# Kernel tuning notes

Hardware: AMD Instinct MI355X
Metric: run time of the kernel (lower is better)

Reference implementation:

```python
import jax, jax.numpy as jnp
import numpy as np

H_STEP = 0.1  # diffusion step size h


def vector_layer(V, W):
    """V: [B, Cin, 9, N]; W: [Cout, Cin, 6].
    Faithful to torch vectorLayer: per component-group, conv1d with kernel
    covering the 3 group entries == contraction over (Cin, group), then the
    scalar result is broadcast back to the 3 group positions.
    Groups [0,3,6]->W[:,:,:3], [1,4,7]->W[:,:,3:6], [2,5,8]->W[:,:,3:6]."""
    o0 = jnp.einsum('bcgn,ocg->bon', V[:, :, (0, 3, 6), :], W[:, :, 0:3])
    o1 = jnp.einsum('bcgn,ocg->bon', V[:, :, (1, 4, 7), :], W[:, :, 3:6])
    o2 = jnp.einsum('bcgn,ocg->bon', V[:, :, (2, 5, 8), :], W[:, :, 3:6])
    S = jnp.stack([o0, o1, o2], axis=2)          # [B, Cout, 3, N]
    return jnp.tile(S, (1, 1, 3, 1))             # positions i get o_{i%3}


def vector_relu(V, Q):
    """Projection ReLU. V: [B, C, 9, N] viewed as [B, C, 3, 3(xyz), N];
    subtract the ReLU'd projection onto direction Q per 3-vector."""
    B, C, _, N = V.shape
    V5 = V.reshape(B, C, 3, 3, N)
    qnorm = jnp.linalg.norm(Q)
    Qb = (Q / qnorm)[None, None, None, :, None]
    T = jnp.sum(V5 * Q[None, None, None, :, None], axis=3, keepdims=True)
    W = V5 - jax.nn.relu(T / qnorm) * Qb
    return W.reshape(B, C, 9, N)


def double_vector_layer(x, K1, K2, Q):
    x = vector_relu(x, Q)
    x = vector_layer(x, K1)
    x = vector_relu(x, Q)
    x = vector_layer(x, K2)
    return vector_relu(x, Q)


def setup_inputs() -> dict:
    key = jax.random.key(0)
    ks = jax.random.split(key, 12)
    N, E = 8192, 65536
    nNin, nEin, nNopen, nEopen, nNclose, nlayer = 3, 1, 16, 1, 3, 5
    nopen = nNopen + 2 * nEopen   # 18
    nhid = 2 * nopen              # 36
    s = 0.05  # kernel scale for numerical stability over 5 layers
    return {
        'xnV': jax.random.normal(ks[0], (1, nNin, 9, N), jnp.float32),
        'xeV': jax.random.normal(ks[1], (1, nEin, 9, E), jnp.float32),
        'iInd': jax.random.randint(ks[2], (E,), 0, N),
        'jInd': jax.random.randint(ks[3], (E,), 0, N),
        'K1Nopen': s * jax.random.normal(ks[4], (nNopen, nNin, 6), jnp.float32),
        'K2Nopen': s * jax.random.normal(ks[5], (nNopen, nNopen, 6), jnp.float32),
        'K1Eopen': s * jax.random.normal(ks[6], (nEopen, nEin, 6), jnp.float32),
        'K2Eopen': s * jax.random.normal(ks[7], (nEopen, nEopen, 6), jnp.float32),
        'KE1': s * jax.random.normal(ks[8], (nlayer, nhid, nhid, 6), jnp.float32),
        'KE2': s * jax.random.normal(ks[9], (nlayer, nhid, nhid, 6), jnp.float32),
        'KNclose': s * jax.random.normal(ks[10], (nNclose, nopen, 6), jnp.float32),
        'Q': jax.random.normal(ks[11], (3,), jnp.float32),
    }


def reference(xnV, xeV, iInd, jInd, K1Nopen, K2Nopen, K1Eopen, K2Eopen,
              KE1, KE2, KNclose, Q):
    N = xnV.shape[-1]
    nopen = K2Nopen.shape[0] + 2 * K2Eopen.shape[0]

    def node_grad(x):   # node -> edge gather difference
        return x[..., iInd] - x[..., jInd]

    def node_ave(x):    # node -> edge gather average
        return 0.5 * (x[..., iInd] + x[..., jInd])

    def edge_div(g):    # edge -> node signed scatter-add
        z = jnp.zeros(g.shape[:-1] + (N,), g.dtype)
        return z.at[..., iInd].add(g).at[..., jInd].add(-g)

    def edge_ave(g):    # edge -> node averaged scatter-add
        z = jnp.zeros(g.shape[:-1] + (N,), g.dtype)
        return 0.5 * z.at[..., iInd].add(g).at[..., jInd].add(g)

    xn = double_vector_layer(xnV, K1Nopen, K2Nopen, Q)   # [1,16,9,N]
    xe = double_vector_layer(xeV, K1Eopen, K2Eopen, Q)   # [1,1,9,E]
    xn = jnp.concatenate([xn, edge_div(xe), edge_ave(xe)], axis=1)  # [1,18,9,N]

    Flux = None
    for i in range(KE1.shape[0]):  # fixed nlayer=5 structurally distinct weights
        dxe = jnp.concatenate([node_grad(xn), node_ave(xn)], axis=1)  # [1,36,9,E]
        Flux = double_vector_layer(dxe, KE1[i], KE2[i], Q)            # [1,36,9,E]
        dxn = edge_div(Flux[:, :nopen]) + edge_ave(Flux[:, nopen:])   # [1,18,9,N]
        xn = xn - H_STEP * dxn

    out = vector_layer(xn, KNclose)  # [1,3,9,N]
    return out, Flux
```

## Files before the change

### kernel.cpp

```cpp
#include <hip/hip_runtime.h>

#define N_NODES 8192
#define N_EDGES 65536
#define NS 56

#define XN3_OFF   0
#define MIT_OFF   (N_NODES*NS)
#define K2N_OFF   (MIT_OFF + 5*5760)
#define KNC_OFF   (K2N_OFF + 2*16*16)
#define K2E_OFF   (KNC_OFF + 2*3*18)
#define FLUX_OFF  488176
#define FLUX_END  (FLUX_OFF + 2*N_EDGES*32)
#define DEG_OFF   FLUX_END
#define RP_OFF    (DEG_OFF + N_NODES)
#define FP_OFF    (RP_OFF + N_NODES + 1)
#define POSI_OFF  (FP_OFF + N_NODES)
#define POSJ_OFF  (POSI_OFF + N_EDGES)

typedef float f32x2 __attribute__((ext_vector_type(2)));
typedef __fp16 fp16x2 __attribute__((ext_vector_type(2)));

__device__ __forceinline__ unsigned pkrtz(float a, float b) {
    fp16x2 h = __builtin_amdgcn_cvt_pkrtz(a, b);
    return *(unsigned*)&h;
}

template<int SLOT>
__device__ __forceinline__ float qb(float x) {
    int r = __builtin_amdgcn_update_dpp(0, __float_as_int(x), SLOT * 0x55, 0xf, 0xf, true);
    return __int_as_float(r);
}
__device__ __forceinline__ float qswap2(float x) {
    int r = __builtin_amdgcn_update_dpp(0, __float_as_int(x), 0x4E, 0xf, 0xf, true);
    return __int_as_float(r);
}

__device__ __forceinline__ void vrelu_p(float& a0, f32x2& a12,
                                        float q0, f32x2 q12, float iq2) {
    float t = fmaf(a0, q0, fmaf(a12.x, q12.x, a12.y * q12.y));
    float r = t > 0.f ? t * iq2 : 0.f;
    a0 = fmaf(-r, q0, a0);
    f32x2 nr = {-r, -r};
    a12 = nr * q12 + a12;
}

__device__ __forceinline__ void vrelu3(float& x0, float& x1, float& x2,
                                       float q0, float q1, float q2, float iq2) {
    float t = x0*q0 + x1*q1 + x2*q2;
    float r = t > 0.f ? t*iq2 : 0.f;
    x0 = fmaf(-r, q0, x0);
    x1 = fmaf(-r, q1, x1);
    x2 = fmaf(-r, q2, x2);
}

template<int QS>
__device__ __forceinline__ void matvec_part(const float* __restrict__ mbase, int q,
        const float (&v0)[9], const f32x2 (&v12)[9],
        f32x2 (&a0p)[4], float& a0s, f32x2 (&a12)[9]) {
    const float* rb = mbase + QS*720 + q*20;
#pragma unroll
    for (int kc = 0; kc < 9; ++kc) {
        float b0 = qb<QS>(v0[kc]);
        f32x2 b12; b12.x = qb<QS>(v12[kc].x); b12.y = qb<QS>(v12[kc].y);
        f32x2 bb0 = {b0, b0};
        const float4* rp = (const float4*)(rb + kc*80);
        float4 R0 = rp[0], R1 = rp[1], R2 = rp[2], R3 = rp[3], R4 = rp[4];
        f32x2 m0p[4] = {{R0.x,R0.y},{R0.z,R0.w},{R1.x,R1.y},{R1.z,R1.w}};
        float mA[9] = {R2.z,R2.w,R3.x,R3.y,R3.z,R3.w,R4.x,R4.y,R4.z};
#pragma unroll
        for (int k = 0; k < 4; ++k) a0p[k] = m0p[k] * bb0 + a0p[k];
        a0s = fmaf(R2.x, b0, a0s);
#pragma unroll
        for (int k = 0; k < 9; ++k) {
            f32x2 mm = {mA[k], mA[k]};
            a12[k] = mm * b12 + a12[k];
        }
    }
}

__global__ void precompute_kernel(const float* __restrict__ K2N,
                                  const float* __restrict__ K2E,
                                  const float* __restrict__ KE1,
                                  const float* __restrict__ KE2,
                                  const float* __restrict__ KNc,
                                  float* __restrict__ ws,
                                  int* __restrict__ deg) {
    int tid = blockIdx.x * blockDim.x + threadIdx.x;
    int nthr = gridDim.x * blockDim.x;
    if (tid < N_NODES) deg[tid] = 0;
    for (int m = tid; m < 1440; m += nthr) {
        ws[MIT_OFF + m*20 + 9]  = 0.f;
        ws[MIT_OFF + m*20 + 19] = 0.f;
    }
    for (int m = tid; m < 5*1296; m += nthr) {
        int l = m / 1296, oc = m % 1296;
        int o = oc / 36, c = oc % 36;
        int qq = o / 9, k = o % 9;
        const float* p1 = KE1 + (size_t)(l*1296 + oc)*6;
        const float* p2 = KE2 + (size_t)(l*1296 + oc)*6;
        int base = MIT_OFF + l*5760 + (c*4 + qq)*20;
        ws[base + k]             = p1[0] + p1[1] + p1[2];
        ws[base + 10 + k]        = p1[3] + p1[4] + p1[5];
        ws[base + 2880 + k]      = p2[0] + p2[1] + p2[2];
        ws[base + 2880 + 10 + k] = p2[3] + p2[4] + p2[5];
    }
    for (int m = tid; m < 2*256; m += nthr) {
        int s = m / 256, oc = m % 256;
        const float* p = K2N + oc*6 + 3*s;
        ws[K2N_OFF + m] = p[0] + p[1] + p[2];
    }
    for (int m = tid; m < 2*54; m += nthr) {
        int s = m / 54, oc = m % 54;
        const float* p = KNc + oc*6 + 3*s;
        ws[KNC_OFF + m] = p[0] + p[1] + p[2];
    }
    if (tid < 2) {
        const float* p = K2E + 3*tid;
        ws[K2E_OFF + tid] = p[0] + p[1] + p[2];
    }
}

__global__ void count_kernel(const int* __restrict__ iInd, const int* __restrict__ jInd,
                             int* __restrict__ deg) {
    int e = blockIdx.x * blockDim.x + threadIdx.x;
    if (e >= N_EDGES) return;
    atomicAdd(&deg[iInd[e]], 1);
    atomicAdd(&deg[jInd[e]], 1);
}

__global__ void scan_kernel(const int* __restrict__ deg, int* __restrict__ rowptr,
                            int* __restrict__ fpos) {
    __shared__ int lds[256];
    int t = threadIdx.x;
    int base = t * 32;
    int s = 0;
#pragma unroll
    for (int k = 0; k < 32; ++k) s += deg[base + k];
    lds[t] = s;
    __syncthreads();
    if (t == 0) {
        int run = 0;
        for (int k = 0; k < 256; ++k) { int v = lds[k]; lds[k] = run; run += v; }
        rowptr[N_NODES] = run;
    }
    __syncthreads();
    int off = lds[t];
#pragma unroll
    for (int k = 0; k < 32; ++k) {
        rowptr[base + k] = off;
        fpos[base + k] = off;
        off += deg[base + k];
    }
}

__global__ void fill_kernel(const int* __restrict__ iInd, const int* __restrict__ jInd,
                            int* __restrict__ fpos,
                            int* __restrict__ posI, int* __restrict__ posJ) {
    int e = blockIdx.x * blockDim.x + threadIdx.x;
    if (e >= N_EDGES) return;
    posI[e] = atomicAdd(&fpos[iInd[e]], 1);
    posJ[e] = atomicAdd(&fpos[jInd[e]], 1);
}

__global__ void open_kernel(const float* __restrict__ xnV,
                            const float* __restrict__ xeV,
                            const float* __restrict__ Q,
                            const float* __restrict__ K1N,
                            const float* __restrict__ K1E,
                            const float* __restrict__ ws,
                            const int* __restrict__ posI, const int* __restrict__ posJ,
                            float* __restrict__ xn3,
                            float4* __restrict__ seslot) {
    float q0 = Q[0], q1 = Q[1], q2 = Q[2];
    float iq2 = 1.f / (q0*q0 + q1*q1 + q2*q2);

    if (blockIdx.x < 32) {
        int n = blockIdx.x * 256 + threadIdx.x;
        float R[3][9];
#pragma unroll
        for (int c = 0; c < 3; ++c)
#pragma unroll
            for (int p = 0; p < 9; ++p)
                R[c][p] = xnV[(c*9 + p)*N_NODES + n];
#pragma unroll
        for (int c = 0; c < 3; ++c)
#pragma unroll
            for (int v = 0; v < 3; ++v)
                vrelu3(R[c][3*v], R[c][3*v+1], R[c][3*v+2], q0, q1, q2, iq2);

        float s[16][3];
#pragma unroll
        for (int o = 0; o < 16; ++o) {
            float a0 = 0.f, a1 = 0.f, a2 = 0.f;
#pragma unroll
            for (int c = 0; c < 3; ++c)
#pragma unroll
                for (int g = 0; g < 3; ++g) {
                    a0 = fmaf(R[c][3*g + 0], K1N[(o*3 + c)*6 + g],     a0);
                    a1 = fmaf(R[c][3*g + 1], K1N[(o*3 + c)*6 + 3 + g], a1);
                    a2 = fmaf(R[c][3*g + 2], K1N[(o*3 + c)*6 + 3 + g], a2);
                }
            s[o][0] = a0; s[o][1] = a1; s[o][2] = a2;
        }
#pragma unroll
        for (int o = 0; o < 16; ++o)
            vrelu3(s[o][0], s[o][1], s[o][2], q0, q1, q2, iq2);

        float u[16][3];
#pragma unroll
        for (int o = 0; o < 16; ++o) {
            float a0 = 0.f, a1 = 0.f, a2 = 0.f;
#pragma unroll
            for (int c = 0; c < 16; ++c) {
                float m0 = ws[K2N_OFF + o*16 + c];
                float mA = ws[K2N_OFF + 256 + o*16 + c];
                a0 = fmaf(m0, s[c][0], a0);
                a1 = fmaf(mA, s[c][1], a1);
                a2 = fmaf(mA, s[c][2], a2);
            }
            u[o][0] = a0; u[o][1] = a1; u[o][2] = a2;
            vrelu3(u[o][0], u[o][1], u[o][2], q0, q1, q2, iq2);
        }

        float* dst = xn3 + n*NS;
#pragma unroll
        for (int o = 0; o < 16; ++o) {
            int base = (o/9)*28 + (o%9)*3;
#pragma unroll
            for (int g = 0; g < 3; ++g)
                dst[base + g] = u[o][g];
        }
        dst[27] = 0.f;
    } else {
        int e = (blockIdx.x - 32) * 256 + threadIdx.x;
        float R[9];
#pragma unroll
        for (int p = 0; p < 9; ++p) R[p] = xeV[p*N_EDGES + e];
#pragma unroll
        for (int v = 0; v < 3; ++v)
            vrelu3(R[3*v], R[3*v+1], R[3*v+2], q0, q1, q2, iq2);

        float s0 = 0.f, s1 = 0.f, s2 = 0.f;
#pragma unroll
        for (int g = 0; g < 3; ++g) {
            s0 = fmaf(R[3*g + 0], K1E[g],     s0);
            s1 = fmaf(R[3*g + 1], K1E[3 + g], s1);
            s2 = fmaf(R[3*g + 2], K1E[3 + g], s2);
        }
        vrelu3(s0, s1, s2, q0, q1, q2, iq2);
        s0 *= ws[K2E_OFF + 0];
        s1 *= ws[K2E_OFF + 1];
        s2 *= ws[K2E_OFF + 1];
        vrelu3(s0, s1, s2, q0, q1, q2, iq2);

        seslot[posI[e]] = make_float4( s0,  s1,  s2,  1.f);
        seslot[posJ[e]] = make_float4(-s0, -s1, -s2, -1.f);
    }
}

__global__ void open_gather_kernel(const float4* __restrict__ seslot,
                                   const int* __restrict__ rowptr,
                                   float* __restrict__ xn3) {
    int n = blockIdx.x * blockDim.x + threadIdx.x;
    if (n >= N_NODES) return;
    int beg = rowptr[n], end = rowptr[n + 1];
    float d0 = 0.f, d1 = 0.f, d2 = 0.f, a0 = 0.f, a1 = 0.f, a2 = 0.f;
    for (int d = beg; d < end; ++d) {
        float4 v = seslot[d];
        d0 += v.x; d1 += v.y; d2 += v.z;
        float hs = 0.5f * v.w;
        a0 = fmaf(hs, v.x, a0); a1 = fmaf(hs, v.y, a1); a2 = fmaf(hs, v.z, a2);
    }
    float* dst = xn3 + n*NS;
    dst[49] = d0; dst[50] = d1; dst[51] = d2;
    dst[52] = a0; dst[53] = a1; dst[54] = a2;
    dst[55] = 0.f;
}

template<bool WRITE_FLUX>
__global__ __launch_bounds__(256, 2) void edge_compute_kernel(
        const float* __restrict__ xn3,
        const int* __restrict__ iInd, const int* __restrict__ jInd,
        const int* __restrict__ posI, const int* __restrict__ posJ,
        const float* __restrict__ Q,
        const float* __restrict__ mitg,
        unsigned* __restrict__ flux16, float* __restrict__ fluxOut) {
    __shared__ float mit[5760];
    {
        const float4* s4 = (const float4*)mitg;
        float4* d4 = (float4*)mit;
        for (int t = threadIdx.x; t < 1440; t += 256) d4[t] = s4[t];
    }
    __syncthreads();

    int tid = blockIdx.x * 256 + threadIdx.x;
    int e = tid >> 2, q = tid & 3;
    float q0 = Q[0];
    f32x2 q12 = {Q[1], Q[2]};
    float iq2 = 1.f / (q0*q0 + q12.x*q12.x + q12.y*q12.y);
    int i = iInd[e], j = jInd[e];
    const float4* xi = (const float4*)(xn3 + i*NS + 28*(q & 1));
    const float4* xj = (const float4*)(xn3 + j*NS + 28*(q & 1));

    bool isAve = q >= 2;
    float sA = isAve ? 0.5f :  1.f;
    float sB = isAve ? 0.5f : -1.f;

    float vv[28];
#pragma unroll
    for (int t = 0; t < 7; ++t) {
        float4 a = xi[t], b = xj[t];
        vv[4*t+0] = fmaf(sA, a.x, sB * b.x);
        vv[4*t+1] = fmaf(sA, a.y, sB * b.y);
        vv[4*t+2] = fmaf(sA, a.z, sB * b.z);
        vv[4*t+3] = fmaf(sA, a.w, sB * b.w);
    }

    float v0[9]; f32x2 v12[9];
#pragma unroll
    for (int k = 0; k < 9; ++k) {
        v0[k]    = vv[3*k];
        v12[k].x = vv[3*k+1];
        v12[k].y = vv[3*k+2];
        vrelu_p(v0[k], v12[k], q0, q12, iq2);
    }

    f32x2 a0p[4]; float a0s; f32x2 a12[9];
#pragma unroll
    for (int k = 0; k < 4; ++k) a0p[k] = (f32x2){0.f, 0.f};
    a0s = 0.f;
#pragma unroll
    for (int k = 0; k < 9; ++k) a12[k] = (f32x2){0.f, 0.f};
    matvec_part<0>(mit, q, v0, v12, a0p, a0s, a12);
    matvec_part<1>(mit, q, v0, v12, a0p, a0s, a12);
    matvec_part<2>(mit, q, v0, v12, a0p, a0s, a12);
    matvec_part<3>(mit, q, v0, v12, a0p, a0s, a12);
#pragma unroll
    for (int k = 0; k < 9; ++k) {
        float w0 = (k < 8) ? ((k & 1) ? a0p[k>>1].y : a0p[k>>1].x) : a0s;
        f32x2 w12 = a12[k];
        vrelu_p(w0, w12, q0, q12, iq2);
        v0[k] = w0; v12[k] = w12;
    }
#pragma unroll
    for (int k = 0; k < 4; ++k) a0p[k] = (f32x2){0.f, 0.f};
    a0s = 0.f;
#pragma unroll
    for (int k = 0; k < 9; ++k) a12[k] = (f32x2){0.f, 0.f};
    matvec_part<0>(mit + 2880, q, v0, v12, a0p, a0s, a12);
    matvec_part<1>(mit + 2880, q, v0, v12, a0p, a0s, a12);
    matvec_part<2>(mit + 2880, q, v0, v12, a0p, a0s, a12);
    matvec_part<3>(mit + 2880, q, v0, v12, a0p, a0s, a12);

    float w0[9]; f32x2 w12[9];
#pragma unroll
    for (int k = 0; k < 9; ++k) {
        w0[k] = (k < 8) ? ((k & 1) ? a0p[k>>1].y : a0p[k>>1].x) : a0s;
        w12[k] = a12[k];
        vrelu_p(w0[k], w12[k], q0, q12, iq2);
    }

    float selO = (q < 2) ? 1.f  : 0.5f;
    float selP = (q < 2) ? 0.5f : -1.f;
    float outv[27];
#pragma unroll
    for (int k = 0; k < 9; ++k) {
        float o0 = qswap2(w0[k]);
        float o1 = qswap2(w12[k].x);
        float o2 = qswap2(w12[k].y);
        outv[3*k]   = fmaf(selO, w0[k],    selP * o0);
        outv[3*k+1] = fmaf(selO, w12[k].x, selP * o1);
        outv[3*k+2] = fmaf(selO, w12[k].y, selP * o2);
    }
    unsigned pk[16];
#pragma unroll
    for (int t = 0; t < 13; ++t) pk[t] = pkrtz(outv[2*t], outv[2*t+1]);
    pk[13] = pkrtz(outv[26], 0.f);
    pk[14] = 0u; pk[15] = 0u;
    int slot = (q < 2) ? posI[e] : posJ[e];
    uint4* dst = (uint4*)(flux16 + (size_t)slot*32 + (q & 1)*16);
    dst[0] = make_uint4(pk[0],  pk[1],  pk[2],  pk[3]);
    dst[1] = make_uint4(pk[4],  pk[5],  pk[6],  pk[7]);
    dst[2] = make_uint4(pk[8],  pk[9],  pk[10], pk[11]);
    dst[3] = make_uint4(pk[12], pk[13], pk[14], pk[15]);

    if (WRITE_FLUX) {
#pragma unroll
        for (int k = 0; k < 9; ++k) {
#pragma unroll
            for (int p = 0; p < 9; ++p) {
                float wv = (p % 3 == 0) ? w0[k] : (p % 3 == 1) ? w12[k].x : w12[k].y;
                fluxOut[((size_t)((9*q + k)*9 + p))*N_EDGES + e] = wv;
            }
        }
    }
}

__global__ __launch_bounds__(64) void node_gather_kernel(
        const __fp16* __restrict__ flux16,
        const int* __restrict__ rowptr,
        float* __restrict__ xn3) {
    int n = blockIdx.x;
    int l = threadIdx.x;
    int beg = rowptr[n], end = rowptr[n + 1];
    const __fp16* p = flux16 + (size_t)beg * 64 + l;
    float acc = 0.f, acc2 = 0.f;
    int d = beg;
    for (; d + 2 <= end; d += 2) {
        acc  += (float)p[0];
        acc2 += (float)p[64];
        p += 128;
    }
    if (d < end) acc += (float)p[0];
    acc += acc2;
    int m = l & 31;
    if (m < 27) {
        float* x = xn3 + n*NS + (l >> 5)*28 + m;
        *x = fmaf(-0.1f, acc, *x);
    }
}

__global__ void close_kernel(const float* __restrict__ xn3,
                             const float* __restrict__ ws,
                             float* __restrict__ out) {
    int n = blockIdx.x * blockDim.x + threadIdx.x;
    if (n >= N_NODES) return;
    const float* x = xn3 + n*NS;
    float o[3][3];
#pragma unroll
    for (int oo = 0; oo < 3; ++oo) {
        float a0 = 0.f, a1 = 0.f, a2 = 0.f;
#pragma unroll
        for (int c = 0; c < 18; ++c) {
            int xidx = (c/9)*28 + (c%9)*3;
            float m0 = ws[KNC_OFF + oo*18 + c];
            float mA = ws[KNC_OFF + 54 + oo*18 + c];
            a0 = fmaf(m0, x[xidx + 0], a0);
            a1 = fmaf(mA, x[xidx + 1], a1);
            a2 = fmaf(mA, x[xidx + 2], a2);
        }
        o[oo][0] = a0; o[oo][1] = a1; o[oo][2] = a2;
    }
#pragma unroll
    for (int oo = 0; oo < 3; ++oo)
#pragma unroll
        for (int p = 0; p < 9; ++p)
            out[(oo*9 + p)*N_NODES + n] = o[oo][p % 3];
}

extern "C" void kernel_launch(void* const* d_in, const int* in_sizes, int n_in,
                              void* d_out, int out_size, void* d_ws, size_t ws_size,
                              hipStream_t stream) {
    const float* xnV = (const float*)d_in[0];
    const float* xeV = (const float*)d_in[1];
    const int*   iInd = (const int*)d_in[2];
    const int*   jInd = (const int*)d_in[3];
    const float* K1N = (const float*)d_in[4];
    const float* K2N = (const float*)d_in[5];
    const float* K1E = (const float*)d_in[6];
    const float* K2E = (const float*)d_in[7];
    const float* KE1 = (const float*)d_in[8];
    const float* KE2 = (const float*)d_in[9];
    const float* KNc = (const float*)d_in[10];
    const float* Q   = (const float*)d_in[11];

    float* ws   = (float*)d_ws;
    float* xn3  = ws + XN3_OFF;
    unsigned* flux16 = (unsigned*)(ws + FLUX_OFF);
    float4* se4 = (float4*)(ws + FLUX_OFF);
    int* wsi    = (int*)d_ws;
    int* deg    = wsi + DEG_OFF;
    int* rowptr = wsi + RP_OFF;
    int* fpos   = wsi + FP_OFF;
    int* posI   = wsi + POSI_OFF;
    int* posJ   = wsi + POSJ_OFF;

    float* out  = (float*)d_out;
    float* fluxOut = out + 3*9*N_NODES;

    precompute_kernel<<<64, 256, 0, stream>>>(K2N, K2E, KE1, KE2, KNc, ws, deg);
    count_kernel<<<N_EDGES/256, 256, 0, stream>>>(iInd, jInd, deg);
    scan_kernel<<<1, 256, 0, stream>>>(deg, rowptr, fpos);
    fill_kernel<<<N_EDGES/256, 256, 0, stream>>>(iInd, jInd, fpos, posI, posJ);

    open_kernel<<<32 + N_EDGES/256, 256, 0, stream>>>(
        xnV, xeV, Q, K1N, K1E, ws, posI, posJ, xn3, se4);
    open_gather_kernel<<<N_NODES/256, 256, 0, stream>>>(se4, rowptr, xn3);

    for (int l = 0; l < 5; ++l) {
        const float* mitg = ws + MIT_OFF + l*5760;
        if (l == 4)
            edge_compute_kernel<true><<<N_EDGES*4/256, 256, 0, stream>>>(
                xn3, iInd, jInd, posI, posJ, Q, mitg, flux16, fluxOut);
        else
            edge_compute_kernel<false><<<N_EDGES*4/256, 256, 0, stream>>>(
                xn3, iInd, jInd, posI, posJ, Q, mitg, flux16, nullptr);
        node_gather_kernel<<<N_NODES, 64, 0, stream>>>((const __fp16*)flux16, rowptr, xn3);
    }

    close_kernel<<<N_NODES/256, 256, 0, stream>>>(xn3, ws, out);
}
```

Before: 280.8 us.

## Process two edges per thread in edge kernel and pad node stride to 64

Each thread in the edge compute kernel now handles two edges, so every shared-memory weight load is reused for both, and the grid is halved. The node state row stride grows from 56 to 64 floats with halves aligned at 32, which simplifies node_gather indexing and aligns the gathers. The cost is roughly double the register pressure per thread under launch_bounds(256,2), which may cause spills or lower occupancy, and half as many threads are available to hide the gather latency.

```diff
diff --git a/kernel.cpp b/kernel.cpp
--- a/kernel.cpp
+++ b/kernel.cpp
@@ -2,14 +2,14 @@
 
 #define N_NODES 8192
 #define N_EDGES 65536
-#define NS 56
+#define NS 64
 
 #define XN3_OFF   0
 #define MIT_OFF   (N_NODES*NS)
 #define K2N_OFF   (MIT_OFF + 5*5760)
 #define KNC_OFF   (K2N_OFF + 2*16*16)
 #define K2E_OFF   (KNC_OFF + 2*3*18)
-#define FLUX_OFF  488176
+#define FLUX_OFF  553728
 #define FLUX_END  (FLUX_OFF + 2*N_EDGES*32)
 #define DEG_OFF   FLUX_END
 #define RP_OFF    (DEG_OFF + N_NODES)
@@ -54,26 +54,36 @@
 }
 
 template<int QS>
-__device__ __forceinline__ void matvec_part(const float* __restrict__ mbase, int q,
-        const float (&v0)[9], const f32x2 (&v12)[9],
-        f32x2 (&a0p)[4], float& a0s, f32x2 (&a12)[9]) {
+__device__ __forceinline__ void matvec2(const float* __restrict__ mbase, int q,
+        const float (&v0a)[9], const f32x2 (&v12a)[9],
+        const float (&v0b)[9], const f32x2 (&v12b)[9],
+        f32x2 (&a0pa)[4], float& a0sa, f32x2 (&a12a)[9],
+        f32x2 (&a0pb)[4], float& a0sb, f32x2 (&a12b)[9]) {
     const float* rb = mbase + QS*720 + q*20;
 #pragma unroll
     for (int kc = 0; kc < 9; ++kc) {
-        float b0 = qb<QS>(v0[kc]);
-        f32x2 b12; b12.x = qb<QS>(v12[kc].x); b12.y = qb<QS>(v12[kc].y);
-        f32x2 bb0 = {b0, b0};
+        float b0a = qb<QS>(v0a[kc]);
+        f32x2 b12a; b12a.x = qb<QS>(v12a[kc].x); b12a.y = qb<QS>(v12a[kc].y);
+        float b0b = qb<QS>(v0b[kc]);
+        f32x2 b12b; b12b.x = qb<QS>(v12b[kc].x); b12b.y = qb<QS>(v12b[kc].y);
+        f32x2 bb0a = {b0a, b0a};
+        f32x2 bb0b = {b0b, b0b};
         const float4* rp = (const float4*)(rb + kc*80);
         float4 R0 = rp[0], R1 = rp[1], R2 = rp[2], R3 = rp[3], R4 = rp[4];
         f32x2 m0p[4] = {{R0.x,R0.y},{R0.z,R0.w},{R1.x,R1.y},{R1.z,R1.w}};
         float mA[9] = {R2.z,R2.w,R3.x,R3.y,R3.z,R3.w,R4.x,R4.y,R4.z};
 #pragma unroll
-        for (int k = 0; k < 4; ++k) a0p[k] = m0p[k] * bb0 + a0p[k];
-        a0s = fmaf(R2.x, b0, a0s);
+        for (int k = 0; k < 4; ++k) {
+            a0pa[k] = m0p[k] * bb0a + a0pa[k];
+            a0pb[k] = m0p[k] * bb0b + a0pb[k];
+        }
+        a0sa = fmaf(R2.x, b0a, a0sa);
+        a0sb = fmaf(R2.x, b0b, a0sb);
 #pragma unroll
         for (int k = 0; k < 9; ++k) {
             f32x2 mm = {mA[k], mA[k]};
-            a12[k] = mm * b12 + a12[k];
+            a12a[k] = mm * b12a + a12a[k];
+            a12b[k] = mm * b12b + a12b[k];
         }
     }
 }
@@ -225,12 +235,13 @@
         float* dst = xn3 + n*NS;
 #pragma unroll
         for (int o = 0; o < 16; ++o) {
-            int base = (o/9)*28 + (o%9)*3;
+            int base = (o/9)*32 + (o%9)*3;
 #pragma unroll
             for (int g = 0; g < 3; ++g)
                 dst[base + g] = u[o][g];
         }
-        dst[27] = 0.f;
+#pragma unroll
+        for (int k = 27; k < 32; ++k) dst[k] = 0.f;
     } else {
         int e = (blockIdx.x - 32) * 256 + threadIdx.x;
         float R[9];
@@ -272,9 +283,10 @@
         a0 = fmaf(hs, v.x, a0); a1 = fmaf(hs, v.y, a1); a2 = fmaf(hs, v.z, a2);
     }
     float* dst = xn3 + n*NS;
-    dst[49] = d0; dst[50] = d1; dst[51] = d2;
-    dst[52] = a0; dst[53] = a1; dst[54] = a2;
-    dst[55] = 0.f;
+    dst[53] = d0; dst[54] = d1; dst[55] = d2;
+    dst[56] = a0; dst[57] = a1; dst[58] = a2;
+#pragma unroll
+    for (int k = 59; k < 64; ++k) dst[k] = 0.f;
 }
 
 template<bool WRITE_FLUX>
@@ -294,103 +306,148 @@
     __syncthreads();
 
     int tid = blockIdx.x * 256 + threadIdx.x;
-    int e = tid >> 2, q = tid & 3;
+    int qd = tid >> 2, q = tid & 3;
+    int e0 = qd << 1, e1 = e0 | 1;
     float q0 = Q[0];
     f32x2 q12 = {Q[1], Q[2]};
     float iq2 = 1.f / (q0*q0 + q12.x*q12.x + q12.y*q12.y);
-    int i = iInd[e], j = jInd[e];
-    const float4* xi = (const float4*)(xn3 + i*NS + 28*(q & 1));
-    const float4* xj = (const float4*)(xn3 + j*NS + 28*(q & 1));
+    int hofs = 32*(q & 1);
+    const float4* xi0 = (const float4*)(xn3 + iInd[e0]*NS + hofs);
+    const float4* xj0 = (const float4*)(xn3 + jInd[e0]*NS + hofs);
+    const float4* xi1 = (const float4*)(xn3 + iInd[e1]*NS + hofs);
+    const float4* xj1 = (const float4*)(xn3 + jInd[e1]*NS + hofs);
 
     bool isAve = q >= 2;
     float sA = isAve ? 0.5f :  1.f;
     float sB = isAve ? 0.5f : -1.f;
 
-    float vv[28];
+    float vvA[28], vvB[28];
 #pragma unroll
     for (int t = 0; t < 7; ++t) {
-        float4 a = xi[t], b = xj[t];
-        vv[4*t+0] = fmaf(sA, a.x, sB * b.x);
-        vv[4*t+1] = fmaf(sA, a.y, sB * b.y);
-        vv[4*t+2] = fmaf(sA, a.z, sB * b.z);
-        vv[4*t+3] = fmaf(sA, a.w, sB * b.w);
-    }
-
-    float v0[9]; f32x2 v12[9];
+        float4 a = xi0[t], b = xj0[t];
+        vvA[4*t+0] = fmaf(sA, a.x, sB * b.x);
+        vvA[4*t+1] = fmaf(sA, a.y, sB * b.y);
+        vvA[4*t+2] = fmaf(sA, a.z, sB * b.z);
+        vvA[4*t+3] = fmaf(sA, a.w, sB * b.w);
+        float4 c = xi1[t], d = xj1[t];
+        vvB[4*t+0] = fmaf(sA, c.x, sB * d.x);
+        vvB[4*t+1] = fmaf(sA, c.y, sB * d.y);
+        vvB[4*t+2] = fmaf(sA, c.z, sB * d.z);
+        vvB[4*t+3] = fmaf(sA, c.w, sB * d.w);
+    }
+
+    float v0a[9], v0b[9]; f32x2 v12a[9], v12b[9];
 #pragma unroll
     for (int k = 0; k < 9; ++k) {
-        v0[k]    = vv[3*k];
-        v12[k].x = vv[3*k+1];
-        v12[k].y = vv[3*k+2];
-        vrelu_p(v0[k], v12[k], q0, q12, iq2);
-    }
-
-    f32x2 a0p[4]; float a0s; f32x2 a12[9];
-#pragma unroll
-    for (int k = 0; k < 4; ++k) a0p[k] = (f32x2){0.f, 0.f};
-    a0s = 0.f;
-#pragma unroll
-    for (int k = 0; k < 9; ++k) a12[k] = (f32x2){0.f, 0.f};
-    matvec_part<0>(mit, q, v0, v12, a0p, a0s, a12);
-    matvec_part<1>(mit, q, v0, v12, a0p, a0s, a12);
-    matvec_part<2>(mit, q, v0, v12, a0p, a0s, a12);
-    matvec_part<3>(mit, q, v0, v12, a0p, a0s, a12);
+        v0a[k]    = vvA[3*k];
+        v12a[k].x = vvA[3*k+1];
+        v12a[k].y = vvA[3*k+2];
+        vrelu_p(v0a[k], v12a[k], q0, q12, iq2);
+        v0b[k]    = vvB[3*k];
+        v12b[k].x = vvB[3*k+1];
+        v12b[k].y = vvB[3*k+2];
+        vrelu_p(v0b[k], v12b[k], q0, q12, iq2);
+    }
+
+    f32x2 a0pa[4], a0pb[4]; float a0sa, a0sb; f32x2 a12a[9], a12b[9];
+#pragma unroll
+    for (int k = 0; k < 4; ++k) { a0pa[k] = (f32x2){0.f,0.f}; a0pb[k] = (f32x2){0.f,0.f}; }
+    a0sa = 0.f; a0sb = 0.f;
+#pragma unroll
+    for (int k = 0; k < 9; ++k) { a12a[k] = (f32x2){0.f,0.f}; a12b[k] = (f32x2){0.f,0.f}; }
+    matvec2<0>(mit, q, v0a, v12a, v0b, v12b, a0pa, a0sa, a12a, a0pb, a0sb, a12b);
+    matvec2<1>(mit, q, v0a, v12a, v0b, v12b, a0pa, a0sa, a12a, a0pb, a0sb, a12b);
+    matvec2<2>(mit, q, v0a, v12a, v0b, v12b, a0pa, a0sa, a12a, a0pb, a0sb, a12b);
+    matvec2<3>(mit, q, v0a, v12a, v0b, v12b, a0pa, a0sa, a12a, a0pb, a0sb, a12b);
 #pragma unroll
     for (int k = 0; k < 9; ++k) {
-        float w0 = (k < 8) ? ((k & 1) ? a0p[k>>1].y : a0p[k>>1].x) : a0s;
-        f32x2 w12 = a12[k];
+        float w0 = (k < 8) ? ((k & 1) ? a0pa[k>>1].y : a0pa[k>>1].x) : a0sa;
+        f32x2 w12 = a12a[k];
         vrelu_p(w0, w12, q0, q12, iq2);
-        v0[k] = w0; v12[k] = w12;
-    }
-#pragma unroll
-    for (int k = 0; k < 4; ++k) a0p[k] = (f32x2){0.f, 0.f};
-    a0s = 0.f;
-#pragma unroll
-    for (int k = 0; k < 9; ++k) a12[k] = (f32x2){0.f, 0.f};
-    matvec_part<0>(mit + 2880, q, v0, v12, a0p, a0s, a12);
-    matvec_part<1>(mit + 2880, q, v0, v12, a0p, a0s, a12);
-    matvec_part<2>(mit + 2880, q, v0, v12, a0p, a0s, a12);
-    matvec_part<3>(mit + 2880, q, v0, v12, a0p, a0s, a12);
-
-    float w0[9]; f32x2 w12[9];
+        v0a[k] = w0; v12a[k] = w12;
+        float u0 = (k < 8) ? ((k & 1) ? a0pb[k>>1].y : a0pb[k>>1].x) : a0sb;
+        f32x2 u12 = a12b[k];
+        vrelu_p(u0, u12, q0, q12, iq2);
+        v0b[k] = u0; v12b[k] = u12;
+    }
+#pragma unroll
+    for (int k = 0; k < 4; ++k) { a0pa[k] = (f32x2){0.f,0.f}; a0pb[k] = (f32x2){0.f,0.f}; }
+    a0sa = 0.f; a0sb = 0.f;
+#pragma unroll
+    for (int k = 0; k < 9; ++k) { a12a[k] = (f32x2){0.f,0.f}; a12b[k] = (f32x2){0.f,0.f}; }
+    matvec2<0>(mit + 2880, q, v0a, v12a, v0b, v12b, a0pa, a0sa, a12a, a0pb, a0sb, a12b);
+    matvec2<1>(mit + 2880, q, v0a, v12a, v0b, v12b, a0pa, a0sa, a12a, a0pb, a0sb, a12b);
+    matvec2<2>(mit + 2880, q, v0a, v12a, v0b, v12b, a0pa, a0sa, a12a, a0pb, a0sb, a12b);
+    matvec2<3>(mit + 2880, q, v0a, v12a, v0b, v12b, a0pa, a0sa, a12a, a0pb, a0sb, a12b);
+
 #pragma unroll
     for (int k = 0; k < 9; ++k) {
-        w0[k] = (k < 8) ? ((k & 1) ? a0p[k>>1].y : a0p[k>>1].x) : a0s;
-        w12[k] = a12[k];
-        vrelu_p(w0[k], w12[k], q0, q12, iq2);
+        float w0 = (k < 8) ? ((k & 1) ? a0pa[k>>1].y : a0pa[k>>1].x) : a0sa;
+        f32x2 w12 = a12a[k];
+        vrelu_p(w0, w12, q0, q12, iq2);
+        v0a[k] = w0; v12a[k] = w12;
+        float u0 = (k < 8) ? ((k & 1) ? a0pb[k>>1].y : a0pb[k>>1].x) : a0sb;
+        f32x2 u12 = a12b[k];
+        vrelu_p(u0, u12, q0, q12, iq2);
+        v0b[k] = u0; v12b[k] = u12;
     }
 
     float selO = (q < 2) ? 1.f  : 0.5f;
     float selP = (q < 2) ? 0.5f : -1.f;
-    float outv[27];
-#pragma unroll
-    for (int k = 0; k < 9; ++k) {
-        float o0 = qswap2(w0[k]);
-        float o1 = qswap2(w12[k].x);
-        float o2 = qswap2(w12[k].y);
-        outv[3*k]   = fmaf(selO, w0[k],    selP * o0);
-        outv[3*k+1] = fmaf(selO, w12[k].x, selP * o1);
-        outv[3*k+2] = fmaf(selO, w12[k].y, selP * o2);
-    }
-    unsigned pk[16];
-#pragma unroll
-    for (int t = 0; t < 13; ++t) pk[t] = pkrtz(outv[2*t], outv[2*t+1]);
-    pk[13] = pkrtz(outv[26], 0.f);
-    pk[14] = 0u; pk[15] = 0u;
-    int slot = (q < 2) ? posI[e] : posJ[e];
-    uint4* dst = (uint4*)(flux16 + (size_t)slot*32 + (q & 1)*16);
-    dst[0] = make_uint4(pk[0],  pk[1],  pk[2],  pk[3]);
-    dst[1] = make_uint4(pk[4],  pk[5],  pk[6],  pk[7]);
-    dst[2] = make_uint4(pk[8],  pk[9],  pk[10], pk[11]);
-    dst[3] = make_uint4(pk[12], pk[13], pk[14], pk[15]);
+    {
+        unsigned pk[16];
+#pragma unroll
+        for (int k = 0; k < 9; ++k) {
+            float o0 = qswap2(v0a[k]);
+            float o1 = qswap2(v12a[k].x);
+            float o2 = qswap2(v12a[k].y);
+            vvA[3*k]   = fmaf(selO, v0a[k],    selP * o0);
+            vvA[3*k+1] = fmaf(selO, v12a[k].x, selP * o1);
+            vvA[3*k+2] = fmaf(selO, v12a[k].y, selP * o2);
+        }
+#pragma unroll
+        for (int t = 0; t < 13; ++t) pk[t] = pkrtz(vvA[2*t], vvA[2*t+1]);
+        pk[13] = pkrtz(vvA[26], 0.f);
+        pk[14] = 0u; pk[15] = 0u;
+        int slot = (q < 2) ? posI[e0] : posJ[e0];
+        uint4* dst = (uint4*)(flux16 + (size_t)slot*32 + (q & 1)*16);
+        dst[0] = make_uint4(pk[0],  pk[1],  pk[2],  pk[3]);
+        dst[1] = make_uint4(pk[4],  pk[5],  pk[6],  pk[7]);
+        dst[2] = make_uint4(pk[8],  pk[9],  pk[10], pk[11]);
+        dst[3] = make_uint4(pk[12], pk[13], pk[14], pk[15]);
+    }
+    {
+        unsigned pk[16];
+#pragma unroll
+        for (int k = 0; k < 9; ++k) {
+            float o0 = qswap2(v0b[k]);
+            float o1 = qswap2(v12b[k].x);
+            float o2 = qswap2(v12b[k].y);
+            vvB[3*k]   = fmaf(selO, v0b[k],    selP * o0);
+            vvB[3*k+1] = fmaf(selO, v12b[k].x, selP * o1);
+            vvB[3*k+2] = fmaf(selO, v12b[k].y, selP * o2);
+        }
+#pragma unroll
+        for (int t = 0; t < 13; ++t) pk[t] = pkrtz(vvB[2*t], vvB[2*t+1]);
+        pk[13] = pkrtz(vvB[26], 0.f);
+        pk[14] = 0u; pk[15] = 0u;
+        int slot = (q < 2) ? posI[e1] : posJ[e1];
+        uint4* dst = (uint4*)(flux16 + (size_t)slot*32 + (q & 1)*16);
+        dst[0] = make_uint4(pk[0],  pk[1],  pk[2],  pk[3]);
+        dst[1] = make_uint4(pk[4],  pk[5],  pk[6],  pk[7]);
+        dst[2] = make_uint4(pk[8],  pk[9],  pk[10], pk[11]);
+        dst[3] = make_uint4(pk[12], pk[13], pk[14], pk[15]);
+    }
 
     if (WRITE_FLUX) {
 #pragma unroll
         for (int k = 0; k < 9; ++k) {
 #pragma unroll
             for (int p = 0; p < 9; ++p) {
-                float wv = (p % 3 == 0) ? w0[k] : (p % 3 == 1) ? w12[k].x : w12[k].y;
-                fluxOut[((size_t)((9*q + k)*9 + p))*N_EDGES + e] = wv;
+                float wa = (p % 3 == 0) ? v0a[k] : (p % 3 == 1) ? v12a[k].x : v12a[k].y;
+                fluxOut[((size_t)((9*q + k)*9 + p))*N_EDGES + e0] = wa;
+                float wb = (p % 3 == 0) ? v0b[k] : (p % 3 == 1) ? v12b[k].x : v12b[k].y;
+                fluxOut[((size_t)((9*q + k)*9 + p))*N_EDGES + e1] = wb;
             }
         }
     }
@@ -413,9 +470,8 @@
     }
     if (d < end) acc += (float)p[0];
     acc += acc2;
-    int m = l & 31;
-    if (m < 27) {
-        float* x = xn3 + n*NS + (l >> 5)*28 + m;
+    if ((l & 31) < 27) {
+        float* x = xn3 + n*NS + l;
         *x = fmaf(-0.1f, acc, *x);
     }
 }
@@ -432,7 +488,7 @@
         float a0 = 0.f, a1 = 0.f, a2 = 0.f;
 #pragma unroll
         for (int c = 0; c < 18; ++c) {
-            int xidx = (c/9)*28 + (c%9)*3;
+            int xidx = (c/9)*32 + (c%9)*3;
             float m0 = ws[KNC_OFF + oo*18 + c];
             float mA = ws[KNC_OFF + 54 + oo*18 + c];
             a0 = fmaf(m0, x[xidx + 0], a0);
@@ -490,10 +546,10 @@
     for (int l = 0; l < 5; ++l) {
         const float* mitg = ws + MIT_OFF + l*5760;
         if (l == 4)
-            edge_compute_kernel<true><<<N_EDGES*4/256, 256, 0, stream>>>(
+            edge_compute_kernel<true><<<N_EDGES*2/256, 256, 0, stream>>>(
                 xn3, iInd, jInd, posI, posJ, Q, mitg, flux16, fluxOut);
         else
-            edge_compute_kernel<false><<<N_EDGES*4/256, 256, 0, stream>>>(
+            edge_compute_kernel<false><<<N_EDGES*2/256, 256, 0, stream>>>(
                 xn3, iInd, jInd, posI, posJ, Q, mitg, flux16, nullptr);
         node_gather_kernel<<<N_NODES, 64, 0, stream>>>((const __fp16*)flux16, rowptr, xn3);
     }
```

New measurement: 269.0 us. 4.2% less time.
